# Optimization experiments

Hardware: AMD Instinct MI355X
Metric: run time of the kernel (lower is better)

The kernel has to match this reference:

```python
import jax, jax.numpy as jnp
import numpy as np

B, C, H, W = 1024, 256, 16, 16  # must satisfy H*W == C per the module's bmm(v, attn)


def setup_inputs() -> dict:
    key = jax.random.key(0)
    ks = jax.random.split(key, 8)
    s = 1.0 / np.sqrt(C)
    return {
        "x": jax.random.normal(ks[0], (B, C, H, W), dtype=jnp.float32),
        "Wq": jax.random.normal(ks[1], (C, C), dtype=jnp.float32) * s,
        "bq": jax.random.normal(ks[2], (C,), dtype=jnp.float32) * s,
        "Wk": jax.random.normal(ks[3], (C, C), dtype=jnp.float32) * s,
        "bk": jax.random.normal(ks[4], (C,), dtype=jnp.float32) * s,
        "Wv": jax.random.normal(ks[5], (C, C), dtype=jnp.float32) * s,
        "bv": jax.random.normal(ks[6], (C,), dtype=jnp.float32) * s,
        "gamma": jax.random.normal(ks[7], (1,), dtype=jnp.float32),
    }


def reference(x, Wq, bq, Wk, bk, Wv, bv, gamma):
    b, c, h, w = x.shape
    n = h * w  # equals c by construction

    def conv1x1(Wt, bt):
        # 1x1 conv == per-pixel channel GEMM
        return jnp.einsum('oi,bihw->bohw', Wt, x) + bt[None, :, None, None]

    q = conv1x1(Wq, bq).reshape(b, c, n)            # (B, C, N)
    k = conv1x1(Wk, bk).reshape(b, c, n)            # (B, C, N)
    v = conv1x1(Wv, bv).reshape(b, c, n)            # (B, C, N)

    # attn = bmm(q, k^T) / sqrt(C) -> (B, C, C); softmax over last dim
    scale = jnp.asarray(1.0 / np.sqrt(c), dtype=x.dtype)
    attn = jax.nn.softmax(jnp.einsum('bcn,bdn->bcd', q, k) * scale, axis=-1)

    # out = bmm(v, attn): (B, C, N=C) @ (B, C, C) -> (B, C, C), reshape to (B,C,H,W)
    out = jnp.einsum('bcn,bnd->bcd', v, attn).reshape(b, c, h, w)
    return gamma * out + x
```

## Files before the change

### kernel.cpp

```cpp
#include <hip/hip_runtime.h>


typedef __attribute__((ext_vector_type(8))) short bf16x8;
typedef __attribute__((ext_vector_type(4))) short bf16x4;
typedef __attribute__((ext_vector_type(4))) float f32x4;

#define MFMA16(a, b, c) __builtin_amdgcn_mfma_f32_16x16x32_bf16((a), (b), (c), 0, 0, 0)

#define GLDS16(g, l)                                                      \
  __builtin_amdgcn_global_load_lds(                                       \
      (const __attribute__((address_space(1))) void*)(g),                 \
      (__attribute__((address_space(3))) void*)(l), 16, 0, 0)

static __device__ __forceinline__ unsigned short f2bf(float f) {
  unsigned int u = __float_as_uint(f);
  u += 0x7fffu + ((u >> 16) & 1u);
  return (unsigned short)(u >> 16);
}

static __device__ __forceinline__ int swz(int row, int byteInRow) {
  return row * 512 + (byteInRow ^ ((row & 7) << 4));
}

__global__ void k_prep(const float* __restrict__ Wq, const float* __restrict__ bq,
                       const float* __restrict__ Wk, const float* __restrict__ bk,
                       const float* __restrict__ Wv, const float* __restrict__ bv,
                       const float* __restrict__ gamma,
                       unsigned short* __restrict__ W3h, float* __restrict__ b3) {
  const int r = blockIdx.x;
  const int p = r >> 8, sr = r & 255;
  const float s = (p == 0) ? 0.0625f : (p == 1 ? 1.0f : gamma[0]);
  const float* W = (p == 0) ? Wq : (p == 1 ? Wk : Wv);
  const float* bs = (p == 0) ? bq : (p == 1 ? bk : bv);
  W3h[r * 256 + threadIdx.x] = f2bf(W[sr * 256 + threadIdx.x] * s);
  if (threadIdx.x == 0) b3[r] = bs[sr] * s;
}

__global__ void k_transpose(const float* __restrict__ x, unsigned short* __restrict__ xt) {
  __shared__ float tile[64][65];
  const int b = blockIdx.x;
  const float* xb = x + (size_t)b * 65536;
  unsigned short* xtb = xt + (size_t)b * 65536;
  const int t = threadIdx.x, tx = t & 63, ty = t >> 6;
  const int cp = t & 31, rb = t >> 5;
  for (int tb = 0; tb < 16; ++tb) {
    const int c0 = (tb >> 2) * 64, n0 = (tb & 3) * 64;
    __syncthreads();
#pragma unroll
    for (int yy = 0; yy < 16; ++yy) {
      const int r = ty + yy * 4;
      tile[r][tx] = xb[(c0 + r) * 256 + n0 + tx];
    }
    __syncthreads();
#pragma unroll
    for (int yy = 0; yy < 8; ++yy) {
      const int nl = rb + yy * 8;
      ushort2 v;
      v.x = f2bf(tile[2 * cp][nl]);
      v.y = f2bf(tile[2 * cp + 1][nl]);
      *(ushort2*)(xtb + (n0 + nl) * 256 + c0 + 2 * cp) = v;
    }
  }
}

__global__ __launch_bounds__(256, 4) void k_gemm(
    const unsigned short* __restrict__ W3h, const float* __restrict__ b3,
    const unsigned short* __restrict__ Xt, unsigned short* __restrict__ Y) {
  __shared__ char smem[32768];
  const int bid = blockIdx.x;
  const int swzb = (bid & 7) * 1536 + (bid >> 3);
  const int r_t = swzb % 6, bn_t = swzb / 6;
  const int m0 = r_t * 128, n0 = bn_t * 128;
  const int tid = threadIdx.x, wv = tid >> 6, lane = tid & 63;
  const int lo = lane & 15, hi = lane >> 4;
  const int wm = wv >> 1, wn = wv & 1;

  f32x4 acc[4][4];
#pragma unroll
  for (int i = 0; i < 4; ++i)
#pragma unroll
    for (int j = 0; j < 4; ++j) acc[i][j] = (f32x4){0.f, 0.f, 0.f, 0.f};

  for (int k0 = 0; k0 < 256; k0 += 64) {
#pragma unroll
    for (int j = 0; j < 4; ++j) {
      const int s = j * 256 + tid;
      const int row = s >> 3, gs = (s & 7) ^ (row & 7);
      GLDS16(W3h + (size_t)(m0 + row) * 256 + k0 + gs * 8,
             smem + j * 4096 + wv * 1024);
    }
#pragma unroll
    for (int j = 0; j < 4; ++j) {
      const int s = j * 256 + tid;
      const int row = s >> 3, gs = (s & 7) ^ (row & 7);
      GLDS16(Xt + (size_t)(n0 + row) * 256 + k0 + gs * 8,
             smem + 16384 + j * 4096 + wv * 1024);
    }
    __syncthreads();
#pragma unroll
    for (int kk = 0; kk < 2; ++kk) {
      bf16x8 a[4], b[4];
#pragma unroll
      for (int rt = 0; rt < 4; ++rt) {
        const int row = wm * 64 + rt * 16 + lo, g = kk * 4 + hi;
        a[rt] = *(const bf16x8*)(smem + row * 128 + ((g ^ (row & 7)) * 16));
      }
#pragma unroll
      for (int ct = 0; ct < 4; ++ct) {
        const int row = wn * 64 + ct * 16 + lo, g = kk * 4 + hi;
        b[ct] = *(const bf16x8*)(smem + 16384 + row * 128 + ((g ^ (row & 7)) * 16));
      }
#pragma unroll
      for (int rt = 0; rt < 4; ++rt)
#pragma unroll
        for (int ct = 0; ct < 4; ++ct) acc[rt][ct] = MFMA16(a[rt], b[ct], acc[rt][ct]);
    }
    __syncthreads();
  }

  float b3v[4][4];
#pragma unroll
  for (int rt = 0; rt < 4; ++rt)
#pragma unroll
    for (int reg = 0; reg < 4; ++reg)
      b3v[rt][reg] = b3[m0 + wm * 64 + rt * 16 + hi * 4 + reg];
#pragma unroll
  for (int rt = 0; rt < 4; ++rt)
#pragma unroll
    for (int ct = 0; ct < 4; ++ct)
#pragma unroll
      for (int reg = 0; reg < 4; ++reg) {
        const int m = wm * 64 + rt * 16 + hi * 4 + reg;
        const int n = wn * 64 + ct * 16 + lo;
        *(unsigned short*)(smem + m * 256 + ((n * 2) ^ ((m & 7) << 4))) =
            f2bf(acc[rt][ct][reg] + b3v[rt][reg]);
      }
  __syncthreads();
  const int p = m0 >> 8, sr0 = m0 & 255;
  const int bb = n0 >> 8, nl0 = n0 & 255;
  unsigned short* dstb = Y + (size_t)bb * 196608 + (size_t)p * 65536;
#pragma unroll
  for (int j = 0; j < 8; ++j) {
    const int s = j * 256 + tid;
    const int m = s >> 4, pp = s & 15;
    const int ng = pp ^ (m & 7);
    int4 v = *(const int4*)(smem + m * 256 + pp * 16);
    *(int4*)(dstb + (size_t)(sr0 + m) * 256 + nl0 + ng * 8) = v;
  }
}

__global__ __launch_bounds__(512, 2) void attn4(
    const float* __restrict__ x, const unsigned short* __restrict__ Y,
    float* __restrict__ out) {
  __shared__ char smem[131072];
  const int b = blockIdx.x;
  const float* xb = x + (size_t)b * 65536;
  const unsigned short* Qb = Y + (size_t)b * 196608;
  const unsigned short* Kb = Qb + 65536;
  const unsigned short* Vb = Qb + 131072;
  const int tid = threadIdx.x, w = tid >> 6, lane = tid & 63;
  const int lo = lane & 15, hi = lane >> 4;
  const int r0 = w * 32;

#pragma unroll
  for (int i = 0; i < 16; ++i) {
    const int idx = i * 512 + tid;
    const int row = idx >> 5, c16 = idx & 31;
    const int gs = (c16 & 24) | ((c16 ^ row) & 7);
    GLDS16(Kb + (size_t)row * 256 + gs * 8, smem + idx * 16);
  }
  bf16x8 aq[2][8];
#pragma unroll
  for (int k0 = 0; k0 < 8; ++k0)
#pragma unroll
    for (int rt = 0; rt < 2; ++rt)
      aq[rt][k0] =
          *(const bf16x8*)(Qb + (size_t)(r0 + rt * 16 + lo) * 256 + k0 * 32 + hi * 8);
  __syncthreads();

  {
    f32x4 acc[2][16];
#pragma unroll
    for (int i = 0; i < 2; ++i)
#pragma unroll
      for (int j = 0; j < 16; ++j) acc[i][j] = (f32x4){0.f, 0.f, 0.f, 0.f};
#pragma unroll
    for (int k0 = 0; k0 < 8; ++k0)
#pragma unroll
      for (int ct = 0; ct < 16; ++ct) {
        bf16x8 bb = *(const bf16x8*)(smem + swz(ct * 16 + lo, (k0 * 32 + hi * 8) * 2));
        acc[0][ct] = MFMA16(aq[0][k0], bb, acc[0][ct]);
        acc[1][ct] = MFMA16(aq[1][k0], bb, acc[1][ct]);
      }
#pragma unroll
    for (int rt = 0; rt < 2; ++rt)
#pragma unroll
      for (int reg = 0; reg < 4; ++reg) {
        float s = 0.f;
        float vals[16];
#pragma unroll
        for (int ct = 0; ct < 16; ++ct) {
          const float p = __expf(acc[rt][ct][reg]);
          vals[ct] = p;
          s += p;
        }
        s += __shfl_xor(s, 1);
        s += __shfl_xor(s, 2);
        s += __shfl_xor(s, 4);
        s += __shfl_xor(s, 8);
        const float inv = 1.0f / s;
#pragma unroll
        for (int ct = 0; ct < 16; ++ct) acc[rt][ct][reg] = vals[ct] * inv;
      }
    __syncthreads();
#pragma unroll
    for (int rt = 0; rt < 2; ++rt)
#pragma unroll
      for (int ct = 0; ct < 16; ++ct) {
        const int d = ct * 16 + lo;
        const int s0 = r0 + rt * 16 + hi * 4;
        bf16x4 v;
#pragma unroll
        for (int reg = 0; reg < 4; ++reg) v[reg] = (short)f2bf(acc[rt][ct][reg]);
        *(bf16x4*)(smem + swz(d, s0 * 2)) = v;
      }
  }
  __syncthreads();

  {
    const int rb0 = (w >> 1) * 64, d0 = (w & 1) * 128;
    f32x4 acc[4][8];
#pragma unroll
    for (int i = 0; i < 4; ++i)
#pragma unroll
      for (int j = 0; j < 8; ++j) acc[i][j] = (f32x4){0.f, 0.f, 0.f, 0.f};
    for (int k0 = 0; k0 < 256; k0 += 32) {
      bf16x8 a[4];
#pragma unroll
      for (int rt = 0; rt < 4; ++rt)
        a[rt] = *(const bf16x8*)(Vb + (size_t)(rb0 + rt * 16 + lo) * 256 + k0 + hi * 8);
#pragma unroll
      for (int ct = 0; ct < 8; ++ct) {
        bf16x8 bb = *(const bf16x8*)(smem + swz(d0 + ct * 16 + lo, (k0 + hi * 8) * 2));
#pragma unroll
        for (int rt = 0; rt < 4; ++rt) acc[rt][ct] = MFMA16(a[rt], bb, acc[rt][ct]);
      }
    }
    float* ob = out + (size_t)b * 65536;
#pragma unroll
    for (int rt = 0; rt < 4; ++rt)
#pragma unroll
      for (int reg = 0; reg < 4; ++reg) {
        const int c = rb0 + rt * 16 + hi * 4 + reg;
#pragma unroll
        for (int ct = 0; ct < 8; ++ct) {
          const int d = d0 + ct * 16 + lo;
          const int idx = c * 256 + d;
          ob[idx] = acc[rt][ct][reg] + xb[idx];
        }
      }
  }
}

extern "C" void kernel_launch(void* const* d_in, const int* in_sizes, int n_in,
                              void* d_out, int out_size, void* d_ws, size_t ws_size,
                              hipStream_t stream) {
  const float* x = (const float*)d_in[0];
  const float* Wq = (const float*)d_in[1];
  const float* bq = (const float*)d_in[2];
  const float* Wk = (const float*)d_in[3];
  const float* bk = (const float*)d_in[4];
  const float* Wv = (const float*)d_in[5];
  const float* bv = (const float*)d_in[6];
  const float* gamma = (const float*)d_in[7];
  float* out = (float*)d_out;

  unsigned short* Y = (unsigned short*)d_ws;
  unsigned short* Xt = Y + (size_t)1024 * 196608;
  unsigned short* W3h = Xt + (size_t)1024 * 65536;
  float* b3 = (float*)(W3h + 768 * 256);
  const size_t need = ((size_t)1024 * 196608 + (size_t)1024 * 65536 + 768 * 256) * 2 + 768 * 4;
  if (ws_size < need) return;

  hipLaunchKernelGGL(k_prep, dim3(768), dim3(256), 0, stream,
                     Wq, bq, Wk, bk, Wv, bv, gamma, W3h, b3);
  hipLaunchKernelGGL(k_transpose, dim3(1024), dim3(256), 0, stream, x, Xt);
  hipLaunchKernelGGL(k_gemm, dim3(12288), dim3(256), 0, stream, W3h, b3, Xt, Y);
  hipLaunchKernelGGL(attn4, dim3(1024), dim3(512), 0, stream, x, Y, out);
}
```

Before: 525.1 us.

## Fuse x transpose/bf16 cast into projection GEMM and prefetch V in attention

```diff
diff --git a/kernel.cpp b/kernel.cpp
--- a/kernel.cpp
+++ b/kernel.cpp
@@ -36,44 +36,21 @@
   if (threadIdx.x == 0) b3[r] = bs[sr] * s;
 }
 
-__global__ void k_transpose(const float* __restrict__ x, unsigned short* __restrict__ xt) {
-  __shared__ float tile[64][65];
-  const int b = blockIdx.x;
-  const float* xb = x + (size_t)b * 65536;
-  unsigned short* xtb = xt + (size_t)b * 65536;
-  const int t = threadIdx.x, tx = t & 63, ty = t >> 6;
-  const int cp = t & 31, rb = t >> 5;
-  for (int tb = 0; tb < 16; ++tb) {
-    const int c0 = (tb >> 2) * 64, n0 = (tb & 3) * 64;
-    __syncthreads();
-#pragma unroll
-    for (int yy = 0; yy < 16; ++yy) {
-      const int r = ty + yy * 4;
-      tile[r][tx] = xb[(c0 + r) * 256 + n0 + tx];
-    }
-    __syncthreads();
-#pragma unroll
-    for (int yy = 0; yy < 8; ++yy) {
-      const int nl = rb + yy * 8;
-      ushort2 v;
-      v.x = f2bf(tile[2 * cp][nl]);
-      v.y = f2bf(tile[2 * cp + 1][nl]);
-      *(ushort2*)(xtb + (n0 + nl) * 256 + c0 + 2 * cp) = v;
-    }
-  }
-}
-
-__global__ __launch_bounds__(256, 4) void k_gemm(
+__global__ __launch_bounds__(256, 3) void k_gemm2(
     const unsigned short* __restrict__ W3h, const float* __restrict__ b3,
-    const unsigned short* __restrict__ Xt, unsigned short* __restrict__ Y) {
-  __shared__ char smem[32768];
+    const float* __restrict__ x, unsigned short* __restrict__ Y) {
+  __shared__ char smem[50176];
+  float* TS = (float*)(smem + 32768);
   const int bid = blockIdx.x;
   const int swzb = (bid & 7) * 1536 + (bid >> 3);
   const int r_t = swzb % 6, bn_t = swzb / 6;
   const int m0 = r_t * 128, n0 = bn_t * 128;
+  const int bb = n0 >> 8, nl0 = n0 & 255;
+  const float* xb = x + (size_t)bb * 65536;
   const int tid = threadIdx.x, wv = tid >> 6, lane = tid & 63;
   const int lo = lane & 15, hi = lane >> 4;
   const int wm = wv >> 1, wn = wv & 1;
+  const int tr = tid >> 4, tc = (tid & 15) * 4;
 
   f32x4 acc[4][4];
 #pragma unroll
@@ -89,14 +66,33 @@
       GLDS16(W3h + (size_t)(m0 + row) * 256 + k0 + gs * 8,
              smem + j * 4096 + wv * 1024);
     }
-#pragma unroll
-    for (int j = 0; j < 4; ++j) {
-      const int s = j * 256 + tid;
-      const int row = s >> 3, gs = (s & 7) ^ (row & 7);
-      GLDS16(Xt + (size_t)(n0 + row) * 256 + k0 + gs * 8,
-             smem + 16384 + j * 4096 + wv * 1024);
+    float4 xg[2][4];
+#pragma unroll
+    for (int c = 0; c < 2; ++c)
+#pragma unroll
+      for (int j = 0; j < 4; ++j)
+        xg[c][j] = *(const float4*)(xb + (k0 + tr + j * 16) * 256 + nl0 + c * 64 + tc);
+
+#pragma unroll
+    for (int c = 0; c < 2; ++c) {
+      if (c == 1) __syncthreads();
+#pragma unroll
+      for (int j = 0; j < 4; ++j)
+        *(float4*)(&TS[(tr + j * 16) * 68 + tc]) = xg[c][j];
+      __syncthreads();
+#pragma unroll
+      for (int ff = 0; ff < 2; ++ff) {
+        const int g = wv + ff * 4;
+        const int n = lane;
+        bf16x8 v;
+#pragma unroll
+        for (int j = 0; j < 8; ++j) v[j] = (short)f2bf(TS[(g * 8 + j) * 68 + n]);
+        const int row = c * 64 + n;
+        *(bf16x8*)(smem + 16384 + row * 128 + ((g ^ (row & 7)) * 16)) = v;
+      }
     }
     __syncthreads();
+
 #pragma unroll
     for (int kk = 0; kk < 2; ++kk) {
       bf16x8 a[4], b[4];
@@ -137,7 +133,6 @@
       }
   __syncthreads();
   const int p = m0 >> 8, sr0 = m0 & 255;
-  const int bb = n0 >> 8, nl0 = n0 & 255;
   unsigned short* dstb = Y + (size_t)bb * 196608 + (size_t)p * 65536;
 #pragma unroll
   for (int j = 0; j < 8; ++j) {
@@ -149,7 +144,7 @@
   }
 }
 
-__global__ __launch_bounds__(512, 2) void attn4(
+__global__ __launch_bounds__(512, 2) void attn5(
     const float* __restrict__ x, const unsigned short* __restrict__ Y,
     float* __restrict__ out) {
   __shared__ char smem[131072];
@@ -161,6 +156,7 @@
   const int tid = threadIdx.x, w = tid >> 6, lane = tid & 63;
   const int lo = lane & 15, hi = lane >> 4;
   const int r0 = w * 32;
+  const int rb0 = (w >> 1) * 64, d0 = (w & 1) * 128;
 
 #pragma unroll
   for (int i = 0; i < 16; ++i) {
@@ -178,6 +174,8 @@
           *(const bf16x8*)(Qb + (size_t)(r0 + rt * 16 + lo) * 256 + k0 * 32 + hi * 8);
   __syncthreads();
 
+  bf16x8 av[4][4];
+
   {
     f32x4 acc[2][16];
 #pragma unroll
@@ -192,6 +190,12 @@
         acc[0][ct] = MFMA16(aq[0][k0], bb, acc[0][ct]);
         acc[1][ct] = MFMA16(aq[1][k0], bb, acc[1][ct]);
       }
+#pragma unroll
+    for (int kq = 0; kq < 4; ++kq)
+#pragma unroll
+      for (int rt = 0; rt < 4; ++rt)
+        av[rt][kq] =
+            *(const bf16x8*)(Vb + (size_t)(rb0 + rt * 16 + lo) * 256 + kq * 32 + hi * 8);
 #pragma unroll
     for (int rt = 0; rt < 2; ++rt)
 #pragma unroll
@@ -228,20 +232,28 @@
   __syncthreads();
 
   {
-    const int rb0 = (w >> 1) * 64, d0 = (w & 1) * 128;
     f32x4 acc[4][8];
 #pragma unroll
     for (int i = 0; i < 4; ++i)
 #pragma unroll
       for (int j = 0; j < 8; ++j) acc[i][j] = (f32x4){0.f, 0.f, 0.f, 0.f};
-    for (int k0 = 0; k0 < 256; k0 += 32) {
+#pragma unroll
+    for (int k0 = 0; k0 < 4; ++k0)
+#pragma unroll
+      for (int ct = 0; ct < 8; ++ct) {
+        bf16x8 bb = *(const bf16x8*)(smem + swz(d0 + ct * 16 + lo, (k0 * 32 + hi * 8) * 2));
+#pragma unroll
+        for (int rt = 0; rt < 4; ++rt) acc[rt][ct] = MFMA16(av[rt][k0], bb, acc[rt][ct]);
+      }
+#pragma unroll
+    for (int k0 = 4; k0 < 8; ++k0) {
       bf16x8 a[4];
 #pragma unroll
       for (int rt = 0; rt < 4; ++rt)
-        a[rt] = *(const bf16x8*)(Vb + (size_t)(rb0 + rt * 16 + lo) * 256 + k0 + hi * 8);
+        a[rt] = *(const bf16x8*)(Vb + (size_t)(rb0 + rt * 16 + lo) * 256 + k0 * 32 + hi * 8);
 #pragma unroll
       for (int ct = 0; ct < 8; ++ct) {
-        bf16x8 bb = *(const bf16x8*)(smem + swz(d0 + ct * 16 + lo, (k0 + hi * 8) * 2));
+        bf16x8 bb = *(const bf16x8*)(smem + swz(d0 + ct * 16 + lo, (k0 * 32 + hi * 8) * 2));
 #pragma unroll
         for (int rt = 0; rt < 4; ++rt) acc[rt][ct] = MFMA16(a[rt], bb, acc[rt][ct]);
       }
@@ -276,15 +288,13 @@
   float* out = (float*)d_out;
 
   unsigned short* Y = (unsigned short*)d_ws;
-  unsigned short* Xt = Y + (size_t)1024 * 196608;
-  unsigned short* W3h = Xt + (size_t)1024 * 65536;
+  unsigned short* W3h = Y + (size_t)1024 * 196608;
   float* b3 = (float*)(W3h + 768 * 256);
-  const size_t need = ((size_t)1024 * 196608 + (size_t)1024 * 65536 + 768 * 256) * 2 + 768 * 4;
+  const size_t need = ((size_t)1024 * 196608 + 768 * 256) * 2 + 768 * 4;
   if (ws_size < need) return;
 
   hipLaunchKernelGGL(k_prep, dim3(768), dim3(256), 0, stream,
                      Wq, bq, Wk, bk, Wv, bv, gamma, W3h, b3);
-  hipLaunchKernelGGL(k_transpose, dim3(1024), dim3(256), 0, stream, x, Xt);
-  hipLaunchKernelGGL(k_gemm, dim3(12288), dim3(256), 0, stream, W3h, b3, Xt, Y);
-  hipLaunchKernelGGL(attn4, dim3(1024), dim3(512), 0, stream, x, Y, out);
-}
+  hipLaunchKernelGGL(k_gemm2, dim3(12288), dim3(256), 0, stream, W3h, b3, x, Y);
+  hipLaunchKernelGGL(attn5, dim3(1024), dim3(512), 0, stream, x, Y, out);
+}
```

Result: slower. 847.1 us (+61.3%).

## Use 1024-thread attention blocks with V prefetch overlapping softmax

Applied to the files above, without the earlier changes.

```diff
diff --git a/kernel.cpp b/kernel.cpp
--- a/kernel.cpp
+++ b/kernel.cpp
@@ -149,7 +149,7 @@
   }
 }
 
-__global__ __launch_bounds__(512, 2) void attn4(
+__global__ __launch_bounds__(1024, 1) void attn6(
     const float* __restrict__ x, const unsigned short* __restrict__ Y,
     float* __restrict__ out) {
   __shared__ char smem[131072];
@@ -160,88 +160,95 @@
   const unsigned short* Vb = Qb + 131072;
   const int tid = threadIdx.x, w = tid >> 6, lane = tid & 63;
   const int lo = lane & 15, hi = lane >> 4;
-  const int r0 = w * 32;
-
-#pragma unroll
-  for (int i = 0; i < 16; ++i) {
-    const int idx = i * 512 + tid;
+  const int r0 = w * 16;
+  const int rb0 = (w >> 2) * 64, d0 = (w & 3) * 64;
+
+#pragma unroll
+  for (int i = 0; i < 8; ++i) {
+    const int idx = i * 1024 + tid;
     const int row = idx >> 5, c16 = idx & 31;
     const int gs = (c16 & 24) | ((c16 ^ row) & 7);
     GLDS16(Kb + (size_t)row * 256 + gs * 8, smem + idx * 16);
   }
-  bf16x8 aq[2][8];
+  bf16x8 aq[8];
 #pragma unroll
   for (int k0 = 0; k0 < 8; ++k0)
-#pragma unroll
-    for (int rt = 0; rt < 2; ++rt)
-      aq[rt][k0] =
-          *(const bf16x8*)(Qb + (size_t)(r0 + rt * 16 + lo) * 256 + k0 * 32 + hi * 8);
+    aq[k0] = *(const bf16x8*)(Qb + (size_t)(r0 + lo) * 256 + k0 * 32 + hi * 8);
   __syncthreads();
 
+  bf16x8 av[4][2];
+
   {
-    f32x4 acc[2][16];
-#pragma unroll
-    for (int i = 0; i < 2; ++i)
-#pragma unroll
-      for (int j = 0; j < 16; ++j) acc[i][j] = (f32x4){0.f, 0.f, 0.f, 0.f};
+    f32x4 acc[16];
+#pragma unroll
+    for (int j = 0; j < 16; ++j) acc[j] = (f32x4){0.f, 0.f, 0.f, 0.f};
 #pragma unroll
     for (int k0 = 0; k0 < 8; ++k0)
 #pragma unroll
       for (int ct = 0; ct < 16; ++ct) {
         bf16x8 bb = *(const bf16x8*)(smem + swz(ct * 16 + lo, (k0 * 32 + hi * 8) * 2));
-        acc[0][ct] = MFMA16(aq[0][k0], bb, acc[0][ct]);
-        acc[1][ct] = MFMA16(aq[1][k0], bb, acc[1][ct]);
-      }
-#pragma unroll
-    for (int rt = 0; rt < 2; ++rt)
-#pragma unroll
-      for (int reg = 0; reg < 4; ++reg) {
-        float s = 0.f;
-        float vals[16];
-#pragma unroll
-        for (int ct = 0; ct < 16; ++ct) {
-          const float p = __expf(acc[rt][ct][reg]);
-          vals[ct] = p;
-          s += p;
-        }
-        s += __shfl_xor(s, 1);
-        s += __shfl_xor(s, 2);
-        s += __shfl_xor(s, 4);
-        s += __shfl_xor(s, 8);
-        const float inv = 1.0f / s;
-#pragma unroll
-        for (int ct = 0; ct < 16; ++ct) acc[rt][ct][reg] = vals[ct] * inv;
-      }
-    __syncthreads();
-#pragma unroll
-    for (int rt = 0; rt < 2; ++rt)
+        acc[ct] = MFMA16(aq[k0], bb, acc[ct]);
+      }
+#pragma unroll
+    for (int kq = 0; kq < 2; ++kq)
+#pragma unroll
+      for (int rt = 0; rt < 4; ++rt)
+        av[rt][kq] =
+            *(const bf16x8*)(Vb + (size_t)(rb0 + rt * 16 + lo) * 256 + kq * 32 + hi * 8);
+#pragma unroll
+    for (int reg = 0; reg < 4; ++reg) {
+      float s = 0.f;
+      float vals[16];
 #pragma unroll
       for (int ct = 0; ct < 16; ++ct) {
-        const int d = ct * 16 + lo;
-        const int s0 = r0 + rt * 16 + hi * 4;
-        bf16x4 v;
-#pragma unroll
-        for (int reg = 0; reg < 4; ++reg) v[reg] = (short)f2bf(acc[rt][ct][reg]);
-        *(bf16x4*)(smem + swz(d, s0 * 2)) = v;
-      }
+        const float p = __expf(acc[ct][reg]);
+        vals[ct] = p;
+        s += p;
+      }
+      s += __shfl_xor(s, 1);
+      s += __shfl_xor(s, 2);
+      s += __shfl_xor(s, 4);
+      s += __shfl_xor(s, 8);
+      const float inv = 1.0f / s;
+#pragma unroll
+      for (int ct = 0; ct < 16; ++ct) acc[ct][reg] = vals[ct] * inv;
+    }
+    __syncthreads();
+#pragma unroll
+    for (int ct = 0; ct < 16; ++ct) {
+      const int d = ct * 16 + lo;
+      const int s0 = r0 + hi * 4;
+      bf16x4 v;
+#pragma unroll
+      for (int reg = 0; reg < 4; ++reg) v[reg] = (short)f2bf(acc[ct][reg]);
+      *(bf16x4*)(smem + swz(d, s0 * 2)) = v;
+    }
   }
   __syncthreads();
 
   {
-    const int rb0 = (w >> 1) * 64, d0 = (w & 1) * 128;
-    f32x4 acc[4][8];
+    f32x4 acc[4][4];
 #pragma unroll
     for (int i = 0; i < 4; ++i)
 #pragma unroll
-      for (int j = 0; j < 8; ++j) acc[i][j] = (f32x4){0.f, 0.f, 0.f, 0.f};
-    for (int k0 = 0; k0 < 256; k0 += 32) {
+      for (int j = 0; j < 4; ++j) acc[i][j] = (f32x4){0.f, 0.f, 0.f, 0.f};
+#pragma unroll
+    for (int k0 = 0; k0 < 2; ++k0)
+#pragma unroll
+      for (int ct = 0; ct < 4; ++ct) {
+        bf16x8 bb = *(const bf16x8*)(smem + swz(d0 + ct * 16 + lo, (k0 * 32 + hi * 8) * 2));
+#pragma unroll
+        for (int rt = 0; rt < 4; ++rt) acc[rt][ct] = MFMA16(av[rt][k0], bb, acc[rt][ct]);
+      }
+#pragma unroll
+    for (int k0 = 2; k0 < 8; ++k0) {
       bf16x8 a[4];
 #pragma unroll
       for (int rt = 0; rt < 4; ++rt)
-        a[rt] = *(const bf16x8*)(Vb + (size_t)(rb0 + rt * 16 + lo) * 256 + k0 + hi * 8);
-#pragma unroll
-      for (int ct = 0; ct < 8; ++ct) {
-        bf16x8 bb = *(const bf16x8*)(smem + swz(d0 + ct * 16 + lo, (k0 + hi * 8) * 2));
+        a[rt] = *(const bf16x8*)(Vb + (size_t)(rb0 + rt * 16 + lo) * 256 + k0 * 32 + hi * 8);
+#pragma unroll
+      for (int ct = 0; ct < 4; ++ct) {
+        bf16x8 bb = *(const bf16x8*)(smem + swz(d0 + ct * 16 + lo, (k0 * 32 + hi * 8) * 2));
 #pragma unroll
         for (int rt = 0; rt < 4; ++rt) acc[rt][ct] = MFMA16(a[rt], bb, acc[rt][ct]);
       }
@@ -253,7 +260,7 @@
       for (int reg = 0; reg < 4; ++reg) {
         const int c = rb0 + rt * 16 + hi * 4 + reg;
 #pragma unroll
-        for (int ct = 0; ct < 8; ++ct) {
+        for (int ct = 0; ct < 4; ++ct) {
           const int d = d0 + ct * 16 + lo;
           const int idx = c * 256 + d;
           ob[idx] = acc[rt][ct][reg] + xb[idx];
@@ -286,5 +293,5 @@
                      Wq, bq, Wk, bk, Wv, bv, gamma, W3h, b3);
   hipLaunchKernelGGL(k_transpose, dim3(1024), dim3(256), 0, stream, x, Xt);
   hipLaunchKernelGGL(k_gemm, dim3(12288), dim3(256), 0, stream, W3h, b3, Xt, Y);
-  hipLaunchKernelGGL(attn4, dim3(1024), dim3(512), 0, stream, x, Y, out);
-}
+  hipLaunchKernelGGL(attn6, dim3(1024), dim3(1024), 0, stream, x, Y, out);
+}
```

Result: slower. 542.1 us (+3.2%).

## Halve attention LDS with double-buffered K quarters and split P write

Applied to the files above, without the earlier changes.

```diff
diff --git a/kernel.cpp b/kernel.cpp
--- a/kernel.cpp
+++ b/kernel.cpp
@@ -18,8 +18,15 @@
   return (unsigned short)(u >> 16);
 }
 
+static __device__ __forceinline__ float bf2f(unsigned short s) {
+  return __uint_as_float((unsigned int)s << 16);
+}
+
 static __device__ __forceinline__ int swz(int row, int byteInRow) {
   return row * 512 + (byteInRow ^ ((row & 7) << 4));
+}
+static __device__ __forceinline__ int swz256(int row, int byteInRow) {
+  return row * 256 + (byteInRow ^ ((row & 7) << 4));
 }
 
 __global__ void k_prep(const float* __restrict__ Wq, const float* __restrict__ bq,
@@ -149,10 +156,10 @@
   }
 }
 
-__global__ __launch_bounds__(512, 2) void attn4(
+__global__ __launch_bounds__(512, 2) void attn7(
     const float* __restrict__ x, const unsigned short* __restrict__ Y,
     float* __restrict__ out) {
-  __shared__ char smem[131072];
+  __shared__ char smem[65536];
   const int b = blockIdx.x;
   const float* xb = x + (size_t)b * 65536;
   const unsigned short* Qb = Y + (size_t)b * 196608;
@@ -162,13 +169,19 @@
   const int lo = lane & 15, hi = lane >> 4;
   const int r0 = w * 32;
 
-#pragma unroll
-  for (int i = 0; i < 16; ++i) {
-    const int idx = i * 512 + tid;
-    const int row = idx >> 5, c16 = idx & 31;
-    const int gs = (c16 & 24) | ((c16 ^ row) & 7);
-    GLDS16(Kb + (size_t)row * 256 + gs * 8, smem + idx * 16);
-  }
+#define STAGE_K(q, reg)                                                     \
+  {                                                                         \
+    _Pragma("unroll") for (int i = 0; i < 4; ++i) {                         \
+      const int idx = i * 512 + tid;              \
+      const int row = idx >> 5, c16 = idx & 31;                             \
+      const int gs = (c16 & 24) | ((c16 ^ row) & 7);                        \
+      GLDS16(Kb + (size_t)((q) * 64 + row) * 256 + gs * 8,                  \
+             smem + (reg) * 32768 + idx * 16);                              \
+    }                                                                       \
+  }
+
+  STAGE_K(0, 0)
+  STAGE_K(1, 1)
   bf16x8 aq[2][8];
 #pragma unroll
   for (int k0 = 0; k0 < 8; ++k0)
@@ -178,88 +191,123 @@
           *(const bf16x8*)(Qb + (size_t)(r0 + rt * 16 + lo) * 256 + k0 * 32 + hi * 8);
   __syncthreads();
 
-  {
-    f32x4 acc[2][16];
-#pragma unroll
-    for (int i = 0; i < 2; ++i)
-#pragma unroll
-      for (int j = 0; j < 16; ++j) acc[i][j] = (f32x4){0.f, 0.f, 0.f, 0.f};
-#pragma unroll
-    for (int k0 = 0; k0 < 8; ++k0)
-#pragma unroll
-      for (int ct = 0; ct < 16; ++ct) {
-        bf16x8 bb = *(const bf16x8*)(smem + swz(ct * 16 + lo, (k0 * 32 + hi * 8) * 2));
-        acc[0][ct] = MFMA16(aq[0][k0], bb, acc[0][ct]);
-        acc[1][ct] = MFMA16(aq[1][k0], bb, acc[1][ct]);
+  bf16x4 pk[4][2][4];
+  f32x4 lsum[2];
+  lsum[0] = (f32x4){0.f, 0.f, 0.f, 0.f};
+  lsum[1] = (f32x4){0.f, 0.f, 0.f, 0.f};
+
+#define QUARTER(q, reg)                                                     \
+  {                                                                         \
+    const char* base = smem + (reg) * 32768;                                \
+    f32x4 acc[2][4];                                                        \
+    _Pragma("unroll") for (int i = 0; i < 2; ++i)                           \
+        _Pragma("unroll") for (int j = 0; j < 4; ++j)                       \
+            acc[i][j] = (f32x4){0.f, 0.f, 0.f, 0.f};                        \
+    _Pragma("unroll") for (int k0 = 0; k0 < 8; ++k0)                        \
+        _Pragma("unroll") for (int ct = 0; ct < 4; ++ct) {                  \
+      bf16x8 bb = *(const bf16x8*)(base + swz(ct * 16 + lo,                 \
+                                              (k0 * 32 + hi * 8) * 2));     \
+      acc[0][ct] = MFMA16(aq[0][k0], bb, acc[0][ct]);                       \
+      acc[1][ct] = MFMA16(aq[1][k0], bb, acc[1][ct]);                       \
+    }                                                                       \
+    _Pragma("unroll") for (int rt = 0; rt < 2; ++rt)                        \
+        _Pragma("unroll") for (int ct = 0; ct < 4; ++ct) {                  \
+      f32x4 p;                                                              \
+      _Pragma("unroll") for (int reg2 = 0; reg2 < 4; ++reg2)                \
+          p[reg2] = __expf(acc[rt][ct][reg2]);                              \
+      lsum[rt] += p;                                                        \
+      bf16x4 v;                                                             \
+      _Pragma("unroll") for (int reg2 = 0; reg2 < 4; ++reg2)                \
+          v[reg2] = (short)f2bf(p[reg2]);                                   \
+      pk[q][rt][ct] = v;                                                    \
+    }                                                                       \
+  }
+
+  QUARTER(0, 0)
+  __syncthreads();
+  STAGE_K(2, 0)
+  QUARTER(1, 1)
+  __syncthreads();
+  STAGE_K(3, 1)
+  QUARTER(2, 0)
+  __syncthreads();
+  QUARTER(3, 1)
+
+  f32x4 inv[2];
+#pragma unroll
+  for (int rt = 0; rt < 2; ++rt)
+#pragma unroll
+    for (int reg = 0; reg < 4; ++reg) {
+      float s = lsum[rt][reg];
+      s += __shfl_xor(s, 1);
+      s += __shfl_xor(s, 2);
+      s += __shfl_xor(s, 4);
+      s += __shfl_xor(s, 8);
+      inv[rt][reg] = 1.0f / s;
+    }
+  __syncthreads();
+
+#define WRITE_PK                                                            \
+  {                                                                         \
+    _Pragma("unroll") for (int q = 0; q < 4; ++q)                           \
+        _Pragma("unroll") for (int rt = 0; rt < 2; ++rt)                    \
+            _Pragma("unroll") for (int ct = 0; ct < 4; ++ct) {              \
+      const int d = q * 64 + ct * 16 + lo;                                  \
+      const int cl = (w & 3) * 32 + rt * 16 + hi * 4;                       \
+      bf16x4 src = pk[q][rt][ct];                                           \
+      bf16x4 v;                                                             \
+      _Pragma("unroll") for (int reg2 = 0; reg2 < 4; ++reg2)                \
+          v[reg2] = (short)f2bf(bf2f((unsigned short)src[reg2]) *           \
+                                inv[rt][reg2]);                             \
+      *(bf16x4*)(smem + swz256(d, cl * 2)) = v;                             \
+    }                                                                       \
+  }
+
+  const int rb0 = (w >> 1) * 64, d0 = (w & 1) * 128;
+  f32x4 accB[4][8];
+#pragma unroll
+  for (int i = 0; i < 4; ++i)
+#pragma unroll
+    for (int j = 0; j < 8; ++j) accB[i][j] = (f32x4){0.f, 0.f, 0.f, 0.f};
+
+#define PV_HALF(h)                                                          \
+  {                                                                         \
+    _Pragma("unroll") for (int k0 = 0; k0 < 4; ++k0) {                      \
+      bf16x8 a[4];                                                          \
+      _Pragma("unroll") for (int rt = 0; rt < 4; ++rt)                      \
+          a[rt] = *(const bf16x8*)(Vb + (size_t)(rb0 + rt * 16 + lo) * 256  \
+                                   + (h) * 128 + k0 * 32 + hi * 8);         \
+      _Pragma("unroll") for (int ct = 0; ct < 8; ++ct) {                    \
+        const int row = d0 + ct * 16 + lo;                                  \
+        bf16x8 bb = *(const bf16x8*)(smem +                                 \
+                                     swz256(row, k0 * 64 + hi * 16));       \
+        _Pragma("unroll") for (int rt = 0; rt < 4; ++rt)                    \
+            accB[rt][ct] = MFMA16(a[rt], bb, accB[rt][ct]);                 \
+      }                                                                     \
+    }                                                                       \
+  }
+
+  if (w < 4) WRITE_PK
+  __syncthreads();
+  PV_HALF(0)
+  __syncthreads();
+  if (w >= 4) WRITE_PK
+  __syncthreads();
+  PV_HALF(1)
+
+  float* ob = out + (size_t)b * 65536;
+#pragma unroll
+  for (int rt = 0; rt < 4; ++rt)
+#pragma unroll
+    for (int reg = 0; reg < 4; ++reg) {
+      const int c = rb0 + rt * 16 + hi * 4 + reg;
+#pragma unroll
+      for (int ct = 0; ct < 8; ++ct) {
+        const int d = d0 + ct * 16 + lo;
+        const int idx = c * 256 + d;
+        ob[idx] = accB[rt][ct][reg] + xb[idx];
       }
-#pragma unroll
-    for (int rt = 0; rt < 2; ++rt)
-#pragma unroll
-      for (int reg = 0; reg < 4; ++reg) {
-        float s = 0.f;
-        float vals[16];
-#pragma unroll
-        for (int ct = 0; ct < 16; ++ct) {
-          const float p = __expf(acc[rt][ct][reg]);
-          vals[ct] = p;
-          s += p;
-        }
-        s += __shfl_xor(s, 1);
-        s += __shfl_xor(s, 2);
-        s += __shfl_xor(s, 4);
-        s += __shfl_xor(s, 8);
-        const float inv = 1.0f / s;
-#pragma unroll
-        for (int ct = 0; ct < 16; ++ct) acc[rt][ct][reg] = vals[ct] * inv;
-      }
-    __syncthreads();
-#pragma unroll
-    for (int rt = 0; rt < 2; ++rt)
-#pragma unroll
-      for (int ct = 0; ct < 16; ++ct) {
-        const int d = ct * 16 + lo;
-        const int s0 = r0 + rt * 16 + hi * 4;
-        bf16x4 v;
-#pragma unroll
-        for (int reg = 0; reg < 4; ++reg) v[reg] = (short)f2bf(acc[rt][ct][reg]);
-        *(bf16x4*)(smem + swz(d, s0 * 2)) = v;
-      }
-  }
-  __syncthreads();
-
-  {
-    const int rb0 = (w >> 1) * 64, d0 = (w & 1) * 128;
-    f32x4 acc[4][8];
-#pragma unroll
-    for (int i = 0; i < 4; ++i)
-#pragma unroll
-      for (int j = 0; j < 8; ++j) acc[i][j] = (f32x4){0.f, 0.f, 0.f, 0.f};
-    for (int k0 = 0; k0 < 256; k0 += 32) {
-      bf16x8 a[4];
-#pragma unroll
-      for (int rt = 0; rt < 4; ++rt)
-        a[rt] = *(const bf16x8*)(Vb + (size_t)(rb0 + rt * 16 + lo) * 256 + k0 + hi * 8);
-#pragma unroll
-      for (int ct = 0; ct < 8; ++ct) {
-        bf16x8 bb = *(const bf16x8*)(smem + swz(d0 + ct * 16 + lo, (k0 + hi * 8) * 2));
-#pragma unroll
-        for (int rt = 0; rt < 4; ++rt) acc[rt][ct] = MFMA16(a[rt], bb, acc[rt][ct]);
-      }
-    }
-    float* ob = out + (size_t)b * 65536;
-#pragma unroll
-    for (int rt = 0; rt < 4; ++rt)
-#pragma unroll
-      for (int reg = 0; reg < 4; ++reg) {
-        const int c = rb0 + rt * 16 + hi * 4 + reg;
-#pragma unroll
-        for (int ct = 0; ct < 8; ++ct) {
-          const int d = d0 + ct * 16 + lo;
-          const int idx = c * 256 + d;
-          ob[idx] = acc[rt][ct][reg] + xb[idx];
-        }
-      }
-  }
+    }
 }
 
 extern "C" void kernel_launch(void* const* d_in, const int* in_sizes, int n_in,
@@ -286,5 +334,5 @@
                      Wq, bq, Wk, bk, Wv, bv, gamma, W3h, b3);
   hipLaunchKernelGGL(k_transpose, dim3(1024), dim3(256), 0, stream, x, Xt);
   hipLaunchKernelGGL(k_gemm, dim3(12288), dim3(256), 0, stream, W3h, b3, Xt, Y);
-  hipLaunchKernelGGL(attn4, dim3(1024), dim3(512), 0, stream, x, Y, out);
-}
+  hipLaunchKernelGGL(attn7, dim3(1024), dim3(512), 0, stream, x, Y, out);
+}
```

Measured after the change: 843.1 us. 60.5% more time.
